# Kernel optimization log

Hardware: AMD Instinct MI355X
Metric: run time of the kernel (lower is better)

## Reference

```python
import jax, jax.numpy as jnp
import numpy as np

EPS = 1e-4   # synsin-style z clamp in world_to_view
BIG = 1e10   # z-buffer init


def _xy_grid(h, w):
    xs = jnp.linspace(-1.0, 1.0, w)
    ys = jnp.linspace(-1.0, 1.0, h)
    gy, gx = jnp.meshgrid(ys, xs, indexing='ij')
    return jnp.stack([gx.ravel(), gy.ravel()], 0)  # [2, h*w], NDC pixel rays


def _view_to_world(depth, K_inv, RTinv, xy):
    # depth [B,1,N]; homogeneous coords rows = (x*d, y*d, d, 1)
    proj = jnp.concatenate([xy[None] * depth, depth, jnp.ones_like(depth)], axis=1)  # [B,4,N]
    cam = jnp.einsum('bij,bjn->bin', K_inv, proj)
    return jnp.einsum('bij,bjn->bin', RTinv, cam)  # [B,4,N]


def _world_to_view(world, K, RT):
    cam2 = jnp.einsum('bij,bjn->bin', RT, world)
    xy_proj = jnp.einsum('bij,bjn->bin', K, cam2)
    z = xy_proj[:, 2:3]
    mask = jnp.abs(z) < EPS
    zs = jnp.where(mask, EPS, z)
    sampler = jnp.concatenate([xy_proj[:, 0:2] / zs, z], axis=1)  # [B,3,N]
    return jnp.where(mask, -10.0, sampler)


def _splat_one(sampler, feats, h, w):
    # sampler [3,N] (x,y in NDC, z depth); feats [C,N]. Nearest-pixel z-buffer splat.
    x, y, z = sampler[0], sampler[1], sampler[2]
    n = x.shape[0]
    px = jnp.round((x + 1.0) * 0.5 * (w - 1)).astype(jnp.int32)
    py = jnp.round((y + 1.0) * 0.5 * (h - 1)).astype(jnp.int32)
    valid = (px >= 0) & (px < w) & (py >= 0) & (py < h) & (z > EPS)
    idx = jnp.where(valid, py * w + px, h * w)  # invalid -> dump bucket h*w
    zv = jnp.where(valid, z, BIG)
    zbuf = jnp.full(h * w + 1, BIG, feats.dtype).at[idx].min(zv)
    pid = jnp.where(valid & (zv <= zbuf[idx]), jnp.arange(n, dtype=jnp.int32), n)
    win = jnp.full(h * w + 1, n, jnp.int32).at[idx].min(pid)[: h * w]  # winning point per pixel
    fpad = jnp.concatenate([feats, jnp.zeros((feats.shape[0], 1), feats.dtype)], axis=1)
    out = fpad[:, win].reshape(feats.shape[0], h, w)
    zb = zbuf[: h * w]
    depth = jnp.where(zb < BIG, zb, 0.0).reshape(1, h, w)
    return out, depth


def _project(depths, colors, feats, K, src_RTs, src_RTinvs, dst_RTs, dst_RTinvs):
    B, V, _, Hc, Wc = depths.shape
    _, _, C, Hf, Wf = feats.shape
    sh, sw = Hf / Hc, Wf / Wc
    scale = jnp.array([sw, sh, 1.0, 1.0], depths.dtype)[None, :, None]
    sK = K * scale
    sKinv = jnp.linalg.inv(sK)

    colors_r = jax.image.resize(colors.reshape(B * V, 3, Hc, Wc), (B * V, 3, Hf, Wf),
                                method='linear', antialias=True)
    depths_r = jax.image.resize(depths.reshape(B * V, 1, Hc, Wc), (B * V, 1, Hf, Wf),
                                method='nearest')
    feats_f = feats.reshape(B, V, C, Hf * Wf)
    colors_f = colors_r.reshape(B, V, 3, Hf * Wf)
    depths_f = depths_r.reshape(B, V, 1, Hf * Wf)

    xy = _xy_grid(Hf, Wf)
    dstRT = dst_RTs[:, 0]  # num_outputs == 1
    splat = jax.vmap(lambda s, f: _splat_one(s, f, Hf, Wf))

    results, warped, pdepths = [], [], []
    for i in range(V):  # small fixed number of source views
        world = _view_to_world(depths_f[:, i], sKinv, src_RTinvs[:, i], xy)
        sampler = _world_to_view(world, sK, dstRT)            # [B,3,N]
        src = jnp.concatenate([feats_f[:, i], colors_f[:, i] * 0.5 + 0.5], axis=1)  # [B,C+3,N]
        res, dep = splat(sampler, src)                        # [B,C+3,Hf,Wf], [B,1,Hf,Wf]
        results.append(res[:, :C])
        warped.append(res[:, C:])
        pdepths.append(dep)

    prj_fs = jnp.stack(results, 0)      # [V,B,C,Hf,Wf]
    warped = jnp.stack(warped, 0)       # [V,B,3,Hf,Wf]
    prj_depths = jnp.stack(pdepths, 0)  # [V,B,1,Hf,Wf]
    # forward() permutes prj_fs / prj_depths to [B,V,...]; warped stays [V,B,...]
    return prj_fs.transpose(1, 0, 2, 3, 4), warped, prj_depths.transpose(1, 0, 2, 3, 4)


def setup_inputs() -> dict:
    key = jax.random.key(0)
    k1, k2, k3 = jax.random.split(key, 3)
    B, V, Hc, Wc = 2, 2, 512, 512
    Hf, Wf, C = 256, 256, 64

    depths = jax.random.uniform(k1, (B, V, 1, Hc, Wc), jnp.float32, 1.0, 5.0)
    colors = jax.random.uniform(k2, (B, V, 3, Hc, Wc), jnp.float32, -1.0, 1.0)
    feats = jax.random.normal(k3, (B, V, C, Hf, Wf), jnp.float32)

    K = np.eye(4, dtype=np.float32)  # NDC intrinsic (fx=fy=1, cx=cy=0)
    th = 0.1
    R = np.array([[np.cos(th), 0, np.sin(th), 0.2],
                  [0, 1, 0, 0.0],
                  [-np.sin(th), 0, np.cos(th), 0.1],
                  [0, 0, 0, 1]], dtype=np.float32)
    src_RT = np.eye(4, dtype=np.float32)

    Kb = jnp.asarray(np.tile(K[None], (B, 1, 1)))
    src_RTs = jnp.asarray(np.tile(src_RT[None, None], (B, V, 1, 1)))
    src_RTinvs = src_RTs  # identity
    dst_RTs = jnp.asarray(np.tile(R[None, None], (B, 1, 1, 1)))
    dst_RTinvs = jnp.asarray(np.tile(np.linalg.inv(R)[None, None], (B, 1, 1, 1)))

    return {"depths": depths, "colors": colors, "feats": feats, "K": Kb,
            "src_RTs": src_RTs, "src_RTinvs": src_RTinvs,
            "dst_RTs": dst_RTs, "dst_RTinvs": dst_RTinvs}


def reference(depths, colors, feats, K, src_RTs, src_RTinvs, dst_RTs, dst_RTinvs):
    return _project(depths, colors, feats, K, src_RTs, src_RTinvs, dst_RTs, dst_RTinvs)
```

## Files before the change

### kernel.cpp

```cpp
#include <hip/hip_runtime.h>
#include <stdint.h>

#pragma clang fp contract(off)

namespace {
constexpr int B_ = 2, V_ = 2, HC = 512, WC = 512, HF = 256, WF = 256, CF = 64;
constexpr int NPIX = HF * WF;
constexpr float EPSF = 1e-4f;
constexpr float BIGF = 1e10f;
constexpr int NPT = B_ * V_ * NPIX;
constexpr int NBLK_PT = NPT / 256;
constexpr int RESIZE_BLKS = (B_ * V_ * 3 * NPIX) / 256;
constexpr int TRANSP_BLKS = B_ * V_ * (NPIX / 64);
constexpr size_t WS_BASE = (size_t)NPT * 8 + (size_t)B_ * V_ * 3 * NPIX * 4 + 256;
constexpr size_t TF_BYTES = (size_t)NPT * CF * 4;
}

__device__ __forceinline__ float dot4f(const float* __restrict__ r,
                                       float v0, float v1, float v2, float v3) {
  float t = r[0] * v0;
  t = t + r[1] * v1;
  t = t + r[2] * v2;
  t = t + r[3] * v3;
  return t;
}

__global__ void prep_k(const float* __restrict__ K,
                       const float* __restrict__ colors,
                       const float* __restrict__ feats,
                       float* __restrict__ colr,
                       float* __restrict__ mats,
                       unsigned long long* __restrict__ zwin,
                       float* __restrict__ tf) {
  __shared__ float lds[CF][65];
  int bid = blockIdx.x;
  int nT = (int)gridDim.x - RESIZE_BLKS;
  int t = threadIdx.x;

  if (bid < nT) {
    int bv = bid >> 10;
    int pix0 = (bid & 1023) << 6;
    int sub = t >> 4;
    int l16 = t & 15;
    const float* fb = feats + (size_t)bv * CF * NPIX;
    #pragma unroll
    for (int pass = 0; pass < 4; ++pass) {
      int ch = pass * 16 + sub;
      const float4 v = *(const float4*)(fb + (size_t)ch * NPIX + pix0 + 4 * l16);
      lds[ch][4*l16+0] = v.x; lds[ch][4*l16+1] = v.y;
      lds[ch][4*l16+2] = v.z; lds[ch][4*l16+3] = v.w;
    }
    __syncthreads();
    float* tb = tf + ((size_t)bv * NPIX + pix0) * CF;
    #pragma unroll
    for (int pass = 0; pass < 4; ++pass) {
      int p = pass * 16 + sub;
      float4 w;
      w.x = lds[4*l16+0][p]; w.y = lds[4*l16+1][p];
      w.z = lds[4*l16+2][p]; w.w = lds[4*l16+3][p];
      *(float4*)(tb + (size_t)p * CF + 4 * l16) = w;
    }
    return;
  }

  int g = (bid - nT) * 256 + t;

  if (g < NPT) zwin[g] = ~0ULL;

  if (g < B_) {
    int b = g;
    const float rowscale[4] = {0.5f, 0.5f, 1.0f, 1.0f};
    float sK[16];
    for (int i = 0; i < 4; ++i)
      for (int j = 0; j < 4; ++j)
        sK[i*4+j] = K[b*16 + i*4 + j] * rowscale[i];
    double m[16];
    for (int i = 0; i < 16; ++i) m[i] = (double)sK[i];
    double inv[16];
    inv[0]  =  m[5]*m[10]*m[15] - m[5]*m[11]*m[14] - m[9]*m[6]*m[15] + m[9]*m[7]*m[14] + m[13]*m[6]*m[11] - m[13]*m[7]*m[10];
    inv[4]  = -m[4]*m[10]*m[15] + m[4]*m[11]*m[14] + m[8]*m[6]*m[15] - m[8]*m[7]*m[14] - m[12]*m[6]*m[11] + m[12]*m[7]*m[10];
    inv[8]  =  m[4]*m[9]*m[15]  - m[4]*m[11]*m[13] - m[8]*m[5]*m[15] + m[8]*m[7]*m[13] + m[12]*m[5]*m[11] - m[12]*m[7]*m[9];
    inv[12] = -m[4]*m[9]*m[14]  + m[4]*m[10]*m[13] + m[8]*m[5]*m[14] - m[8]*m[6]*m[13] - m[12]*m[5]*m[10] + m[12]*m[6]*m[9];
    inv[1]  = -m[1]*m[10]*m[15] + m[1]*m[11]*m[14] + m[9]*m[2]*m[15] - m[9]*m[3]*m[14] - m[13]*m[2]*m[11] + m[13]*m[3]*m[10];
    inv[5]  =  m[0]*m[10]*m[15] - m[0]*m[11]*m[14] - m[8]*m[2]*m[15] + m[8]*m[3]*m[14] + m[12]*m[2]*m[11] - m[12]*m[3]*m[10];
    inv[9]  = -m[0]*m[9]*m[15]  + m[0]*m[11]*m[13] + m[8]*m[1]*m[15] - m[8]*m[3]*m[13] - m[12]*m[1]*m[11] + m[12]*m[3]*m[9];
    inv[13] =  m[0]*m[9]*m[14]  - m[0]*m[10]*m[13] - m[8]*m[1]*m[14] + m[8]*m[2]*m[13] + m[12]*m[1]*m[10] - m[12]*m[2]*m[9];
    inv[2]  =  m[1]*m[6]*m[15]  - m[1]*m[7]*m[14]  - m[5]*m[2]*m[15] + m[5]*m[3]*m[14] + m[13]*m[2]*m[7]  - m[13]*m[3]*m[6];
    inv[6]  = -m[0]*m[6]*m[15]  + m[0]*m[7]*m[14]  + m[4]*m[2]*m[15] - m[4]*m[3]*m[14] - m[12]*m[2]*m[7]  + m[12]*m[3]*m[6];
    inv[10] =  m[0]*m[5]*m[15]  - m[0]*m[7]*m[13]  - m[4]*m[1]*m[15] + m[4]*m[3]*m[13] + m[12]*m[1]*m[7]  - m[12]*m[3]*m[5];
    inv[14] = -m[0]*m[5]*m[14]  + m[0]*m[6]*m[13]  + m[4]*m[1]*m[14] - m[4]*m[2]*m[13] - m[12]*m[1]*m[6]  + m[12]*m[2]*m[5];
    inv[3]  = -m[1]*m[6]*m[11]  + m[1]*m[7]*m[10]  + m[5]*m[2]*m[11] - m[5]*m[3]*m[10] - m[9]*m[2]*m[7]   + m[9]*m[3]*m[6];
    inv[7]  =  m[0]*m[6]*m[11]  - m[0]*m[7]*m[10]  - m[4]*m[2]*m[11] + m[4]*m[3]*m[10] + m[8]*m[2]*m[7]   - m[8]*m[3]*m[6];
    inv[11] = -m[0]*m[5]*m[11]  + m[0]*m[7]*m[9]   + m[4]*m[1]*m[11] - m[4]*m[3]*m[9]  - m[8]*m[1]*m[7]   + m[8]*m[3]*m[5];
    inv[15] =  m[0]*m[5]*m[10]  - m[0]*m[6]*m[9]   - m[4]*m[1]*m[10] + m[4]*m[2]*m[9]  + m[8]*m[1]*m[6]   - m[8]*m[2]*m[5];
    double det = m[0]*inv[0] + m[1]*inv[4] + m[2]*inv[8] + m[3]*inv[12];
    double idet = 1.0 / det;
    for (int i = 0; i < 16; ++i) {
      mats[b*32 + i]      = sK[i];
      mats[b*32 + 16 + i] = (float)(inv[i] * idet);
    }
  }

  int pc  = g >> 16;
  int pix = g & (NPIX - 1);
  int y = pix >> 8, x = pix & (WF - 1);
  const float* src = colors + (size_t)pc * HC * WC;
  const float W37 = (float)(3.0 / 7.0), W17 = (float)(1.0 / 7.0);
  float wy[4] = {0.125f, 0.375f, 0.375f, 0.125f};
  float wx[4] = {0.125f, 0.375f, 0.375f, 0.125f};
  if (y == 0)      { wy[0] = 0.f; wy[1] = W37; wy[2] = W37; wy[3] = W17; }
  if (y == HF - 1) { wy[0] = W17; wy[1] = W37; wy[2] = W37; wy[3] = 0.f; }
  if (x == 0)      { wx[0] = 0.f; wx[1] = W37; wx[2] = W37; wx[3] = W17; }
  if (x == WF - 1) { wx[0] = W17; wx[1] = W37; wx[2] = W37; wx[3] = 0.f; }
  int jy0 = 2 * y - 1, jx0 = 2 * x - 1;
  float acc = 0.f;
  #pragma unroll
  for (int ty = 0; ty < 4; ++ty) {
    if (wy[ty] == 0.f) continue;
    int jy = jy0 + ty;
    float rs = 0.f;
    #pragma unroll
    for (int tx = 0; tx < 4; ++tx) {
      if (wx[tx] == 0.f) continue;
      rs = rs + wx[tx] * src[(size_t)jy * WC + (jx0 + tx)];
    }
    acc = acc + wy[ty] * rs;
  }
  colr[g] = acc;
}

__global__ void splat_k(const float* __restrict__ depths,
                        const float* __restrict__ mats,
                        const float* __restrict__ srcRTinv,
                        const float* __restrict__ dstRT,
                        unsigned long long* __restrict__ zwin) {
  int g = blockIdx.x * blockDim.x + threadIdx.x;
  if (g >= NPT) return;
  int bv = g >> 16;
  int n  = g & (NPIX - 1);
  int b  = bv / V_;
  int y = n >> 8, x = n & (WF - 1);
  float d = depths[(size_t)bv * HC * WC + (size_t)(2 * y + 1) * WC + (2 * x + 1)];
  const float step32 = 2.0f / 255.0f;
  float xf = (float)x * step32 - 1.0f;
  float yf = (float)y * step32 - 1.0f;
  float pr0 = xf * d, pr1 = yf * d, pr2 = d, pr3 = 1.0f;
  const float* sK  = mats + b * 32;
  const float* sKi = mats + b * 32 + 16;
  const float* Rs  = srcRTinv + (size_t)bv * 16;
  const float* Rd  = dstRT + (size_t)b * 16;
  float a0 = dot4f(sKi + 0,  pr0, pr1, pr2, pr3);
  float a1 = dot4f(sKi + 4,  pr0, pr1, pr2, pr3);
  float a2 = dot4f(sKi + 8,  pr0, pr1, pr2, pr3);
  float a3 = dot4f(sKi + 12, pr0, pr1, pr2, pr3);
  float w0 = dot4f(Rs + 0,  a0, a1, a2, a3);
  float w1 = dot4f(Rs + 4,  a0, a1, a2, a3);
  float w2 = dot4f(Rs + 8,  a0, a1, a2, a3);
  float w3 = dot4f(Rs + 12, a0, a1, a2, a3);
  float c0 = dot4f(Rd + 0,  w0, w1, w2, w3);
  float c1 = dot4f(Rd + 4,  w0, w1, w2, w3);
  float c2 = dot4f(Rd + 8,  w0, w1, w2, w3);
  float c3 = dot4f(Rd + 12, w0, w1, w2, w3);
  float p0 = dot4f(sK + 0, c0, c1, c2, c3);
  float p1 = dot4f(sK + 4, c0, c1, c2, c3);
  float p2 = dot4f(sK + 8, c0, c1, c2, c3);
  if (!(p2 > EPSF)) return;
  float sx = p0 / p2, sy = p1 / p2;
  float pxf = rintf(((sx + 1.0f) * 0.5f) * 255.0f);
  float pyf = rintf(((sy + 1.0f) * 0.5f) * 255.0f);
  if (!(pxf >= 0.0f && pxf <= 255.0f && pyf >= 0.0f && pyf <= 255.0f)) return;
  int idx = (int)pyf * WF + (int)pxf;
  unsigned zbits = __float_as_uint(p2);
  unsigned long long key = ((unsigned long long)zbits << 32) | (unsigned)n;
  atomicMin(&zwin[(size_t)bv * NPIX + idx], key);
}

__global__ void gatherT_k(const unsigned long long* __restrict__ zwin,
                          const float* __restrict__ tf,
                          const float* __restrict__ colr,
                          float* __restrict__ out0,
                          float* __restrict__ out1,
                          float* __restrict__ out2) {
  int bid = blockIdx.x;
  int grp = bid >> 10;
  int g   = (bid & (NBLK_PT - 1)) * 256 + threadIdx.x;
  int bv  = g >> 16;
  int pix = g & (NPIX - 1);
  unsigned long long key = zwin[g];
  bool hit = (key != ~0ULL);
  int n = (int)(key & 0xffffffffULL);

  if (grp < 4) {
    float4 f[4];
    if (hit) {
      const float4* src =
          (const float4*)(tf + ((size_t)bv * NPIX + n) * CF + grp * 16);
      #pragma unroll
      for (int i = 0; i < 4; ++i) f[i] = src[i];
    } else {
      #pragma unroll
      for (int i = 0; i < 4; ++i) f[i] = make_float4(0.f, 0.f, 0.f, 0.f);
    }
    float* o0 = out0 + (size_t)bv * CF * NPIX + (size_t)(grp * 16) * NPIX + pix;
    const float* fs = (const float*)f;
    #pragma unroll
    for (int c = 0; c < 16; ++c)
      __builtin_nontemporal_store(fs[c], &o0[(size_t)c * NPIX]);
  } else {
    int b = bv >> 1, v = bv & 1;
    const float* cb = colr + (size_t)bv * 3 * NPIX;
    float* o1 = out1 + (size_t)(v * B_ + b) * 3 * NPIX + pix;
    if (hit) {
      float z = __uint_as_float((unsigned)(key >> 32));
      __builtin_nontemporal_store((z < BIGF) ? z : 0.0f, &out2[g]);
      #pragma unroll
      for (int ch = 0; ch < 3; ++ch)
        __builtin_nontemporal_store(cb[(size_t)ch * NPIX + n] * 0.5f + 0.5f,
                                    &o1[(size_t)ch * NPIX]);
    } else {
      __builtin_nontemporal_store(0.0f, &out2[g]);
      #pragma unroll
      for (int ch = 0; ch < 3; ++ch)
        __builtin_nontemporal_store(0.0f, &o1[(size_t)ch * NPIX]);
    }
  }
}

__global__ void gather_k(const unsigned long long* __restrict__ zwin,
                         const float* __restrict__ feats,
                         const float* __restrict__ colr,
                         float* __restrict__ out0,
                         float* __restrict__ out1,
                         float* __restrict__ out2) {
  int bid = blockIdx.x;
  int grp = bid >> 10;
  int g   = (bid & (NBLK_PT - 1)) * 256 + threadIdx.x;
  int bv  = g >> 16;
  int pix = g & (NPIX - 1);
  unsigned long long key = zwin[g];
  bool hit = (key != ~0ULL);
  int n = (int)(key & 0xffffffffULL);

  if (grp < 4) {
    int c0 = grp * 16;
    const float* fb = feats + (size_t)bv * CF * NPIX + (size_t)c0 * NPIX;
    float* o0 = out0 + (size_t)bv * CF * NPIX + (size_t)c0 * NPIX + pix;
    if (hit) {
      #pragma unroll
      for (int c = 0; c < 16; ++c)
        __builtin_nontemporal_store(fb[(size_t)c * NPIX + n], &o0[(size_t)c * NPIX]);
    } else {
      #pragma unroll
      for (int c = 0; c < 16; ++c)
        __builtin_nontemporal_store(0.0f, &o0[(size_t)c * NPIX]);
    }
  } else {
    int b = bv >> 1, v = bv & 1;
    const float* cb = colr + (size_t)bv * 3 * NPIX;
    float* o1 = out1 + (size_t)(v * B_ + b) * 3 * NPIX + pix;
    if (hit) {
      float z = __uint_as_float((unsigned)(key >> 32));
      __builtin_nontemporal_store((z < BIGF) ? z : 0.0f, &out2[g]);
      #pragma unroll
      for (int ch = 0; ch < 3; ++ch)
        __builtin_nontemporal_store(cb[(size_t)ch * NPIX + n] * 0.5f + 0.5f,
                                    &o1[(size_t)ch * NPIX]);
    } else {
      __builtin_nontemporal_store(0.0f, &out2[g]);
      #pragma unroll
      for (int ch = 0; ch < 3; ++ch)
        __builtin_nontemporal_store(0.0f, &o1[(size_t)ch * NPIX]);
    }
  }
}

extern "C" void kernel_launch(void* const* d_in, const int* in_sizes, int n_in,
                              void* d_out, int out_size, void* d_ws, size_t ws_size,
                              hipStream_t stream) {
  const float* depths     = (const float*)d_in[0];
  const float* colors     = (const float*)d_in[1];
  const float* feats      = (const float*)d_in[2];
  const float* K          = (const float*)d_in[3];
  const float* src_RTinvs = (const float*)d_in[5];
  const float* dst_RTs    = (const float*)d_in[6];

  float* out0 = (float*)d_out;
  float* out1 = out0 + (size_t)B_ * V_ * CF * NPIX;
  float* out2 = out1 + (size_t)V_ * B_ * 3 * NPIX;

  unsigned long long* zwin = (unsigned long long*)d_ws;
  float* colr = (float*)(zwin + NPT);
  float* mats = colr + (size_t)B_ * V_ * 3 * NPIX;
  float* tf   = (float*)((char*)d_ws + WS_BASE);

  const bool use_tf = (ws_size >= WS_BASE + TF_BYTES);

  int prep_grid = use_tf ? (TRANSP_BLKS + RESIZE_BLKS) : RESIZE_BLKS;
  prep_k<<<prep_grid, 256, 0, stream>>>(K, colors, feats, colr, mats, zwin, tf);
  splat_k<<<NBLK_PT, 256, 0, stream>>>(depths, mats, src_RTinvs, dst_RTs, zwin);
  if (use_tf)
    gatherT_k<<<5 * NBLK_PT, 256, 0, stream>>>(zwin, tf, colr, out0, out1, out2);
  else
    gather_k<<<5 * NBLK_PT, 256, 0, stream>>>(zwin, feats, colr, out0, out1, out2);
}
```

Measured before the change: 180.5 us.

## Move feature transpose into splat kernel and drop LDS staging

The feature transpose to pixel-major layout moves out of the prep kernel and into the splat kernel's grid, so it runs alongside the atomic z-buffer splat instead of alongside the color resize. The transpose also drops its LDS tile: each thread now reads four strided channel values directly and writes one float4, using blocks of 16 pixels. This aims to balance work across kernels and remove the shared-memory round trip and barrier. In exchange, the global reads are narrower, each wavefront reading 64-byte segments per channel, which may coalesce worse.

```diff
diff --git a/kernel.cpp b/kernel.cpp
--- a/kernel.cpp
+++ b/kernel.cpp
@@ -11,7 +11,7 @@
 constexpr int NPT = B_ * V_ * NPIX;
 constexpr int NBLK_PT = NPT / 256;
 constexpr int RESIZE_BLKS = (B_ * V_ * 3 * NPIX) / 256;
-constexpr int TRANSP_BLKS = B_ * V_ * (NPIX / 64);
+constexpr int TP_BLKS = B_ * V_ * (NPIX / 16);
 constexpr size_t WS_BASE = (size_t)NPT * 8 + (size_t)B_ * V_ * 3 * NPIX * 4 + 256;
 constexpr size_t TF_BYTES = (size_t)NPT * CF * 4;
 }
@@ -27,43 +27,10 @@
 
 __global__ void prep_k(const float* __restrict__ K,
                        const float* __restrict__ colors,
-                       const float* __restrict__ feats,
                        float* __restrict__ colr,
                        float* __restrict__ mats,
-                       unsigned long long* __restrict__ zwin,
-                       float* __restrict__ tf) {
-  __shared__ float lds[CF][65];
-  int bid = blockIdx.x;
-  int nT = (int)gridDim.x - RESIZE_BLKS;
-  int t = threadIdx.x;
-
-  if (bid < nT) {
-    int bv = bid >> 10;
-    int pix0 = (bid & 1023) << 6;
-    int sub = t >> 4;
-    int l16 = t & 15;
-    const float* fb = feats + (size_t)bv * CF * NPIX;
-    #pragma unroll
-    for (int pass = 0; pass < 4; ++pass) {
-      int ch = pass * 16 + sub;
-      const float4 v = *(const float4*)(fb + (size_t)ch * NPIX + pix0 + 4 * l16);
-      lds[ch][4*l16+0] = v.x; lds[ch][4*l16+1] = v.y;
-      lds[ch][4*l16+2] = v.z; lds[ch][4*l16+3] = v.w;
-    }
-    __syncthreads();
-    float* tb = tf + ((size_t)bv * NPIX + pix0) * CF;
-    #pragma unroll
-    for (int pass = 0; pass < 4; ++pass) {
-      int p = pass * 16 + sub;
-      float4 w;
-      w.x = lds[4*l16+0][p]; w.y = lds[4*l16+1][p];
-      w.z = lds[4*l16+2][p]; w.w = lds[4*l16+3][p];
-      *(float4*)(tb + (size_t)p * CF + 4 * l16) = w;
-    }
-    return;
-  }
-
-  int g = (bid - nT) * 256 + t;
+                       unsigned long long* __restrict__ zwin) {
+  int g = blockIdx.x * blockDim.x + threadIdx.x;
 
   if (g < NPT) zwin[g] = ~0ULL;
 
@@ -101,6 +68,7 @@
     }
   }
 
+  if (g >= B_ * V_ * 3 * NPIX) return;
   int pc  = g >> 16;
   int pix = g & (NPIX - 1);
   int y = pix >> 8, x = pix & (WF - 1);
@@ -129,12 +97,33 @@
   colr[g] = acc;
 }
 
-__global__ void splat_k(const float* __restrict__ depths,
-                        const float* __restrict__ mats,
-                        const float* __restrict__ srcRTinv,
-                        const float* __restrict__ dstRT,
-                        unsigned long long* __restrict__ zwin) {
-  int g = blockIdx.x * blockDim.x + threadIdx.x;
+__global__ void ts_k(const float* __restrict__ depths,
+                     const float* __restrict__ mats,
+                     const float* __restrict__ srcRTinv,
+                     const float* __restrict__ dstRT,
+                     unsigned long long* __restrict__ zwin,
+                     const float* __restrict__ feats,
+                     float* __restrict__ tf) {
+  int bid = blockIdx.x;
+  int nT = (int)gridDim.x - NBLK_PT;
+  int t = threadIdx.x;
+
+  if (bid < nT) {
+    int bv = bid >> 12;
+    int pix0 = (bid & 4095) << 4;
+    int c4 = t >> 4;
+    int p  = t & 15;
+    const float* fb = feats + (size_t)bv * CF * NPIX + pix0 + p;
+    float4 w;
+    w.x = fb[(size_t)(4 * c4 + 0) * NPIX];
+    w.y = fb[(size_t)(4 * c4 + 1) * NPIX];
+    w.z = fb[(size_t)(4 * c4 + 2) * NPIX];
+    w.w = fb[(size_t)(4 * c4 + 3) * NPIX];
+    *(float4*)(tf + ((size_t)bv * NPIX + pix0 + p) * CF + 4 * c4) = w;
+    return;
+  }
+
+  int g = (bid - nT) * 256 + t;
   if (g >= NPT) return;
   int bv = g >> 16;
   int n  = g & (NPIX - 1);
@@ -295,9 +284,9 @@
 
   const bool use_tf = (ws_size >= WS_BASE + TF_BYTES);
 
-  int prep_grid = use_tf ? (TRANSP_BLKS + RESIZE_BLKS) : RESIZE_BLKS;
-  prep_k<<<prep_grid, 256, 0, stream>>>(K, colors, feats, colr, mats, zwin, tf);
-  splat_k<<<NBLK_PT, 256, 0, stream>>>(depths, mats, src_RTinvs, dst_RTs, zwin);
+  prep_k<<<RESIZE_BLKS, 256, 0, stream>>>(K, colors, colr, mats, zwin);
+  int ts_grid = use_tf ? (TP_BLKS + NBLK_PT) : NBLK_PT;
+  ts_k<<<ts_grid, 256, 0, stream>>>(depths, mats, src_RTinvs, dst_RTs, zwin, feats, tf);
   if (use_tf)
     gatherT_k<<<5 * NBLK_PT, 256, 0, stream>>>(zwin, tf, colr, out0, out1, out2);
   else
```

Measured after the change: 188.9 us. 1.05x slower.
